# Performance work log

Measured on AMD Instinct MI355X. Metric: run time of the kernel, lower is better.

The kernel has to match this reference:

```python
import jax, jax.numpy as jnp
import numpy as np

SOS_TOKEN = 1
MAX_LENGTH = 64
VOCAB = 32000
HIDDEN = 1024
BATCH = 32


def setup_inputs() -> dict:
    key = jax.random.key(0)
    ks = jax.random.split(key, 10)
    s = 1.0 / np.sqrt(HIDDEN)
    return {
        "encoder_outputs": jax.random.normal(ks[0], (BATCH, MAX_LENGTH, HIDDEN), dtype=jnp.float32),
        "encoder_hidden": jax.random.normal(ks[1], (1, BATCH, HIDDEN), dtype=jnp.float32),
        "target_tensor": jax.random.randint(ks[2], (BATCH, MAX_LENGTH), 0, VOCAB),
        "embedding": jax.random.normal(ks[3], (VOCAB, HIDDEN), dtype=jnp.float32),
        "W_ih": jax.random.uniform(ks[4], (3 * HIDDEN, HIDDEN), jnp.float32, -s, s),
        "W_hh": jax.random.uniform(ks[5], (3 * HIDDEN, HIDDEN), jnp.float32, -s, s),
        "b_ih": jax.random.uniform(ks[6], (3 * HIDDEN,), jnp.float32, -s, s),
        "b_hh": jax.random.uniform(ks[7], (3 * HIDDEN,), jnp.float32, -s, s),
        "out_W": jax.random.uniform(ks[8], (VOCAB, HIDDEN), jnp.float32, -s, s),
        "out_b": jax.random.uniform(ks[9], (VOCAB,), jnp.float32, -s, s),
    }


def _decode(encoder_hidden, target_tensor, embedding, W_ih, W_hh, b_ih, b_hh, out_W, out_b):
    B = target_tensor.shape[0]
    # teacher forcing: input at step i is SOS (i=0) else target[:, i-1]
    sos = jnp.full((B, 1), SOS_TOKEN, dtype=target_tensor.dtype)
    inputs = jnp.concatenate([sos, target_tensor[:, :-1]], axis=1)  # [B,T]
    x = jax.nn.relu(embedding[inputs])  # [B,T,H]
    # precompute all input-side gate projections in one GEMM: [B,T,3H]
    xg = jnp.einsum("bth,gh->btg", x, W_ih) + b_ih
    h0 = encoder_hidden[0]  # [B,H]

    def step(h, xg_t):
        hg = h @ W_hh.T + b_hh  # [B,3H]
        xr, xz, xn = jnp.split(xg_t, 3, axis=-1)
        hr, hz, hn = jnp.split(hg, 3, axis=-1)
        r = jax.nn.sigmoid(xr + hr)
        z = jax.nn.sigmoid(xz + hz)
        n = jnp.tanh(xn + r * hn)
        h_new = (1.0 - z) * n + z * h
        return h_new, h_new

    h_last, hs = jax.lax.scan(step, h0, jnp.swapaxes(xg, 0, 1))
    hs = jnp.swapaxes(hs, 0, 1)  # [B,T,H]
    logits = jnp.einsum("bth,vh->btv", hs, out_W) + out_b
    log_probs = jax.nn.log_softmax(logits, axis=-1)
    return log_probs, h_last[None]  # hidden shaped [1,B,H] like torch GRU


def reference(encoder_outputs, encoder_hidden, target_tensor, embedding, W_ih, W_hh, b_ih, b_hh, out_W, out_b):
    del encoder_outputs  # only used for batch size in the original
    return _decode(encoder_hidden, target_tensor, embedding, W_ih, W_hh, b_ih, b_hh, out_W, out_b)
```

## Files before the change

### kernel.cpp

```cpp
#include <hip/hip_runtime.h>
#include <hip/hip_bf16.h>

#define B_ 32
#define T_ 64
#define H_ 1024
#define G3 3072
#define V_ 32000
#define M_ 2048
#define NB_SCAN 64
#define NTILE_N 250

typedef __attribute__((ext_vector_type(8))) short s16x8;
typedef __attribute__((ext_vector_type(4))) float f32x4;
typedef __bf16 bf16x8 __attribute__((ext_vector_type(8)));

__device__ inline unsigned short f2bf(float f) {
    union { float f; unsigned int u; } v; v.f = f;
    unsigned int u = v.u;
    return (unsigned short)((u + 0x7FFFu + ((u >> 16) & 1u)) >> 16);
}

__device__ inline s16x8 load_b128_cc(const void* p) {
    s16x8 r;
    asm volatile("global_load_dwordx4 %0, %1, off sc0 sc1" : "=v"(r) : "v"(p));
    return r;
}
__device__ inline unsigned int load_b32_cc(const void* p) {
    unsigned int r;
    asm volatile("global_load_dword %0, %1, off sc0 sc1" : "=v"(r) : "v"(p));
    return r;
}
__device__ inline void store_b32_cc(void* p, unsigned int v) {
    asm volatile("global_store_dword %0, %1, off sc0 sc1" :: "v"(p), "v"(v) : "memory");
}

__global__ __launch_bounds__(256) void prep_all(
    const float* __restrict__ W_ih, const float* __restrict__ W_hh,
    const float* __restrict__ out_W,
    unsigned short* __restrict__ wihb, unsigned short* __restrict__ whhb,
    unsigned short* __restrict__ owb,
    const int* __restrict__ target, const float* __restrict__ emb,
    unsigned short* __restrict__ xb,
    const float* __restrict__ enc_hidden, unsigned short* __restrict__ hb0,
    unsigned int* __restrict__ flg)
{
    int gid = blockIdx.x * 256 + threadIdx.x;
    int gs = gridDim.x * 256;
    const int NW = G3 * H_ / 4;
    const int NO = V_ * H_ / 4;

    for (int i = gid; i < NW; i += gs) {
        float4 v = *(const float4*)(W_ih + (size_t)i * 4);
        ushort4 o; o.x = f2bf(v.x); o.y = f2bf(v.y); o.z = f2bf(v.z); o.w = f2bf(v.w);
        *(ushort4*)(wihb + (size_t)i * 4) = o;
    }
    for (int i = gid; i < NW; i += gs) {
        float4 v = *(const float4*)(W_hh + (size_t)i * 4);
        ushort4 o; o.x = f2bf(v.x); o.y = f2bf(v.y); o.z = f2bf(v.z); o.w = f2bf(v.w);
        *(ushort4*)(whhb + (size_t)i * 4) = o;
    }
    for (int i = gid; i < NO; i += gs) {
        float4 v = *(const float4*)(out_W + (size_t)i * 4);
        ushort4 o; o.x = f2bf(v.x); o.y = f2bf(v.y); o.z = f2bf(v.z); o.w = f2bf(v.w);
        *(ushort4*)(owb + (size_t)i * 4) = o;
    }
    for (int i = gid; i < M_ * 256; i += gs) {
        int m = i >> 8, k = (i & 255) * 4;
        int b = m >> 6, t = m & 63;
        int tok = (t == 0) ? 1 : target[b * T_ + t - 1];
        float4 v = *(const float4*)(emb + (size_t)tok * H_ + k);
        ushort4 o;
        o.x = f2bf(fmaxf(v.x, 0.f)); o.y = f2bf(fmaxf(v.y, 0.f));
        o.z = f2bf(fmaxf(v.z, 0.f)); o.w = f2bf(fmaxf(v.w, 0.f));
        *(ushort4*)(xb + (size_t)m * H_ + k) = o;
    }
    for (int i = gid; i < B_ * H_; i += gs) hb0[i] = f2bf(enc_hidden[i]);
    for (int i = gid; i < 128; i += gs) flg[i] = 0;
}

__global__ __launch_bounds__(256) void gemm_bias(
    const unsigned short* __restrict__ A,
    const unsigned short* __restrict__ Bm,
    const float* __restrict__ bias,
    float* __restrict__ C,
    int N, int K)
{
    __shared__ __align__(16) unsigned short As[3 * 4096];
    __shared__ __align__(16) unsigned short Bs[3 * 4096];
    int n0 = blockIdx.x * 128, m0 = blockIdx.y * 128;
    int tid = threadIdx.x;
    int lane = tid & 63, wv = tid >> 6;
    int wr = wv >> 1, wc = wv & 1;

    f32x4 acc[4][4] = {};

    int o0 = wv * 2048 + lane * 16;
    int row0 = o0 >> 6, sl0 = (o0 >> 4) & 3;
    int ib0 = (sl0 ^ ((row0 >> 1) & 3)) * 8;
    int o1 = o0 + 1024;
    int row1 = o1 >> 6, sl1 = (o1 >> 4) & 3;
    int ib1 = (sl1 ^ ((row1 >> 1) & 3)) * 8;

    auto stage = [&](int buf, int k0) {
        const unsigned short* ga0 = A + (size_t)(m0 + row0) * K + k0 + ib0;
        const unsigned short* gb0 = Bm + (size_t)(n0 + row0) * K + k0 + ib0;
        const unsigned short* ga1 = A + (size_t)(m0 + row1) * K + k0 + ib1;
        const unsigned short* gb1 = Bm + (size_t)(n0 + row1) * K + k0 + ib1;
        unsigned short* la0 = As + buf * 4096 + wv * 1024;
        unsigned short* lb0 = Bs + buf * 4096 + wv * 1024;
        __builtin_amdgcn_global_load_lds((const __attribute__((address_space(1))) void*)ga0,
                                         (__attribute__((address_space(3))) void*)la0, 16, 0, 0);
        __builtin_amdgcn_global_load_lds((const __attribute__((address_space(1))) void*)gb0,
                                         (__attribute__((address_space(3))) void*)lb0, 16, 0, 0);
        __builtin_amdgcn_global_load_lds((const __attribute__((address_space(1))) void*)ga1,
                                         (__attribute__((address_space(3))) void*)(la0 + 512), 16, 0, 0);
        __builtin_amdgcn_global_load_lds((const __attribute__((address_space(1))) void*)gb1,
                                         (__attribute__((address_space(3))) void*)(lb0 + 512), 16, 0, 0);
    };

    int rr2 = lane & 15, q = lane >> 4;
    int kqs = ((q ^ ((rr2 >> 1) & 3)) * 8);
    int rA = wr * 64 + rr2;
    int rB = wc * 64 + rr2;

    int NT = K >> 5;
    stage(0, 0);
    if (NT > 1) {
        stage(1, 32);
        asm volatile("s_waitcnt vmcnt(4)");
    } else {
        asm volatile("s_waitcnt vmcnt(0)");
    }
    __builtin_amdgcn_s_barrier();
    __builtin_amdgcn_sched_barrier(0);

    int cur = 0;
    for (int t = 0; t < NT; ++t) {
        if (t + 2 < NT) {
            int nb = cur + 2; if (nb >= 3) nb -= 3;
            stage(nb, (t + 2) << 5);
        }
        const unsigned short* ab = As + cur * 4096;
        const unsigned short* bb = Bs + cur * 4096;
        s16x8 af[4], bf[4];
#pragma unroll
        for (int i = 0; i < 4; ++i) {
            af[i] = *(const s16x8*)(ab + (rA + i * 16) * 32 + kqs);
            bf[i] = *(const s16x8*)(bb + (rB + i * 16) * 32 + kqs);
        }
#pragma unroll
        for (int mf = 0; mf < 4; ++mf)
#pragma unroll
            for (int nf = 0; nf < 4; ++nf)
                acc[mf][nf] = __builtin_amdgcn_mfma_f32_16x16x32_bf16(
                    __builtin_bit_cast(bf16x8, af[mf]),
                    __builtin_bit_cast(bf16x8, bf[nf]),
                    acc[mf][nf], 0, 0, 0);
        if (t + 1 < NT) {
            if (t + 2 < NT) asm volatile("s_waitcnt vmcnt(4)");
            else            asm volatile("s_waitcnt vmcnt(0)");
            asm volatile("s_waitcnt lgkmcnt(0)");
            __builtin_amdgcn_s_barrier();
            __builtin_amdgcn_sched_barrier(0);
        }
        cur = (cur == 2) ? 0 : cur + 1;
    }

#pragma unroll
    for (int nf = 0; nf < 4; ++nf) {
        int col = n0 + wc * 64 + nf * 16 + rr2;
        float bv = bias[col];
#pragma unroll
        for (int mf = 0; mf < 4; ++mf) {
            int mbase = m0 + wr * 64 + mf * 16 + q * 4;
#pragma unroll
            for (int r = 0; r < 4; ++r)
                C[(size_t)(mbase + r) * N + col] = acc[mf][nf][r] + bv;
        }
    }
}

__global__ __launch_bounds__(256) void gemm_logits(
    const unsigned short* __restrict__ A,
    const unsigned short* __restrict__ Bm,
    const float* __restrict__ bias,
    float* __restrict__ C,
    float* __restrict__ pmax,
    float* __restrict__ psum)
{
    __shared__ __align__(16) unsigned short As[3 * 4096];
    __shared__ __align__(16) unsigned short Bs[3 * 4096];
    __shared__ float spx[2][128], sps[2][128];
    int m0 = blockIdx.x * 128;
    int ntile = blockIdx.y;
    int n0 = ntile * 128;
    int tid = threadIdx.x;
    int lane = tid & 63, wv = tid >> 6;
    int wr = wv >> 1, wc = wv & 1;

    f32x4 acc[4][4] = {};

    int o0 = wv * 2048 + lane * 16;
    int row0 = o0 >> 6, sl0 = (o0 >> 4) & 3;
    int ib0 = (sl0 ^ ((row0 >> 1) & 3)) * 8;
    int o1 = o0 + 1024;
    int row1 = o1 >> 6, sl1 = (o1 >> 4) & 3;
    int ib1 = (sl1 ^ ((row1 >> 1) & 3)) * 8;

    auto stage = [&](int buf, int k0) {
        const unsigned short* ga0 = A + (size_t)(m0 + row0) * H_ + k0 + ib0;
        const unsigned short* gb0 = Bm + (size_t)(n0 + row0) * H_ + k0 + ib0;
        const unsigned short* ga1 = A + (size_t)(m0 + row1) * H_ + k0 + ib1;
        const unsigned short* gb1 = Bm + (size_t)(n0 + row1) * H_ + k0 + ib1;
        unsigned short* la0 = As + buf * 4096 + wv * 1024;
        unsigned short* lb0 = Bs + buf * 4096 + wv * 1024;
        __builtin_amdgcn_global_load_lds((const __attribute__((address_space(1))) void*)ga0,
                                         (__attribute__((address_space(3))) void*)la0, 16, 0, 0);
        __builtin_amdgcn_global_load_lds((const __attribute__((address_space(1))) void*)gb0,
                                         (__attribute__((address_space(3))) void*)lb0, 16, 0, 0);
        __builtin_amdgcn_global_load_lds((const __attribute__((address_space(1))) void*)ga1,
                                         (__attribute__((address_space(3))) void*)(la0 + 512), 16, 0, 0);
        __builtin_amdgcn_global_load_lds((const __attribute__((address_space(1))) void*)gb1,
                                         (__attribute__((address_space(3))) void*)(lb0 + 512), 16, 0, 0);
    };

    int q = lane >> 4, rr2 = lane & 15;
    int kqs = ((q ^ ((rr2 >> 1) & 3)) * 8);
    int rA = wr * 64 + rr2;
    int rB = wc * 64 + rr2;

    stage(0, 0);
    stage(1, 32);
    asm volatile("s_waitcnt vmcnt(4)");
    __builtin_amdgcn_s_barrier();
    __builtin_amdgcn_sched_barrier(0);

    int cur = 0;
    for (int t = 0; t < 32; ++t) {
        if (t + 2 < 32) {
            int nb = cur + 2; if (nb >= 3) nb -= 3;
            stage(nb, (t + 2) << 5);
        }
        const unsigned short* ab = As + cur * 4096;
        const unsigned short* bb = Bs + cur * 4096;
        s16x8 af[4], bf[4];
#pragma unroll
        for (int i = 0; i < 4; ++i) {
            af[i] = *(const s16x8*)(ab + (rA + i * 16) * 32 + kqs);
            bf[i] = *(const s16x8*)(bb + (rB + i * 16) * 32 + kqs);
        }
#pragma unroll
        for (int mf = 0; mf < 4; ++mf)
#pragma unroll
            for (int nf = 0; nf < 4; ++nf)
                acc[mf][nf] = __builtin_amdgcn_mfma_f32_16x16x32_bf16(
                    __builtin_bit_cast(bf16x8, af[mf]),
                    __builtin_bit_cast(bf16x8, bf[nf]),
                    acc[mf][nf], 0, 0, 0);
        if (t + 1 < 32) {
            if (t + 2 < 32) asm volatile("s_waitcnt vmcnt(4)");
            else            asm volatile("s_waitcnt vmcnt(0)");
            asm volatile("s_waitcnt lgkmcnt(0)");
            __builtin_amdgcn_s_barrier();
            __builtin_amdgcn_sched_barrier(0);
        }
        cur = (cur == 2) ? 0 : cur + 1;
    }

    float bv[4];
#pragma unroll
    for (int nf = 0; nf < 4; ++nf) bv[nf] = bias[n0 + wc * 64 + nf * 16 + rr2];

#pragma unroll
    for (int mf = 0; mf < 4; ++mf) {
#pragma unroll
        for (int r = 0; r < 4; ++r) {
            int row_local = wr * 64 + mf * 16 + q * 4 + r;
            float vmax = -1e30f;
#pragma unroll
            for (int nf = 0; nf < 4; ++nf) vmax = fmaxf(vmax, acc[mf][nf][r] + bv[nf]);
#pragma unroll
            for (int o = 1; o < 16; o <<= 1) vmax = fmaxf(vmax, __shfl_xor(vmax, o));
            float vsum = 0.f;
#pragma unroll
            for (int nf = 0; nf < 4; ++nf) vsum += __expf(acc[mf][nf][r] + bv[nf] - vmax);
#pragma unroll
            for (int o = 1; o < 16; o <<= 1) vsum += __shfl_xor(vsum, o);
            if (rr2 == 0) { spx[wc][row_local] = vmax; sps[wc][row_local] = vsum; }
        }
    }

#pragma unroll
    for (int nf = 0; nf < 4; ++nf) {
        int col = n0 + wc * 64 + nf * 16 + rr2;
#pragma unroll
        for (int mf = 0; mf < 4; ++mf) {
            int mbase = m0 + wr * 64 + mf * 16 + q * 4;
#pragma unroll
            for (int r = 0; r < 4; ++r)
                C[(size_t)(mbase + r) * V_ + col] = acc[mf][nf][r] + bv[nf];
        }
    }

    __syncthreads();
    if (wc == 0 && rr2 == 0) {
#pragma unroll
        for (int mf = 0; mf < 4; ++mf)
#pragma unroll
            for (int r = 0; r < 4; ++r) {
                int row_local = wr * 64 + mf * 16 + q * 4 + r;
                float m0v = spx[0][row_local], m1v = spx[1][row_local];
                float Mv = fmaxf(m0v, m1v);
                float Sv = sps[0][row_local] * __expf(m0v - Mv) + sps[1][row_local] * __expf(m1v - Mv);
                pmax[(size_t)(m0 + row_local) * NTILE_N + ntile] = Mv;
                psum[(size_t)(m0 + row_local) * NTILE_N + ntile] = Sv;
            }
    }
}

__global__ __launch_bounds__(256) void gru_scan(
    const unsigned short* __restrict__ Whhb,
    const float* __restrict__ b_hh,
    const float* __restrict__ enc_hidden,
    const float* __restrict__ xg,
    unsigned short* __restrict__ hb0, unsigned short* __restrict__ hb1,
    float* __restrict__ hfF,
    unsigned short* __restrict__ hs,
    unsigned int* __restrict__ flags)
{
    __shared__ __align__(16) unsigned short ws_[48 * 1024];
    __shared__ __align__(16) f32x4 red[2][3][64];

    int tid = threadIdx.x;
    int lane = tid & 63, wave = tid >> 6;
    int rt = wave >> 1, kh = wave & 1;
    int ct = blockIdx.x;

    for (int idx = tid; idx < 48 * 128; idx += 256) {
        int r = idx >> 7, slot = idx & 127;
        int g = r >> 4, jr = r & 15;
        s16x8 v = *(const s16x8*)(Whhb + (size_t)(g * H_ + ct * 16 + jr) * H_ + slot * 8);
        *(s16x8*)(ws_ + r * 1024 + (slot ^ (r & 7)) * 8) = v;
    }
    __syncthreads();

    int rr = lane & 15, q = lane >> 4;
    int col = ct * 16 + rr;
    int xsw = rr & 7;
    int kbase = kh * 512;
    int sbase = kh * 64 + q;
    float br = b_hh[col], bz = b_hh[H_ + col], bn = b_hh[2 * H_ + col];
    int b0 = rt * 16 + q * 4;

    float hold[4];
    float xr[4], xz[4], xn[4];
    if (kh == 1) {
#pragma unroll
        for (int r = 0; r < 4; ++r) {
            hold[r] = enc_hidden[(b0 + r) * H_ + col];
            const float* xrow = xg + ((size_t)(b0 + r) * T_) * G3;
            xr[r] = xrow[col]; xz[r] = xrow[H_ + col]; xn[r] = xrow[2 * H_ + col];
        }
    }

    for (int t = 0; t < T_; ++t) {
        const unsigned short* hbp = (t & 1) ? hb1 : hb0;
        unsigned short*       hbn = (t & 1) ? hb0 : hb1;

        const unsigned short* ha = hbp + (size_t)(rt * 16 + rr) * H_ + kbase + q * 8;
        s16x8 af[16];
#pragma unroll
        for (int i = 0; i < 16; ++i) af[i] = load_b128_cc(ha + i * 32);

        f32x4 accr, accz, accn;
        if (kh == 1) {
            accr = (f32x4){br, br, br, br};
            accz = (f32x4){bz, bz, bz, bz};
            accn = (f32x4){bn, bn, bn, bn};
        } else {
            accr = (f32x4){0.f, 0.f, 0.f, 0.f};
            accz = accr; accn = accr;
        }

        asm volatile("s_waitcnt vmcnt(0)");
        __builtin_amdgcn_sched_barrier(0);

#pragma unroll
        for (int kk = 0; kk < 16; ++kk) {
            int so = ((sbase + kk * 4) ^ xsw) * 8;
            s16x8 fr = *(const s16x8*)(ws_ + rr * 1024 + so);
            s16x8 fz = *(const s16x8*)(ws_ + (16 + rr) * 1024 + so);
            s16x8 fn = *(const s16x8*)(ws_ + (32 + rr) * 1024 + so);
            bf16x8 a = __builtin_bit_cast(bf16x8, af[kk]);
            accr = __builtin_amdgcn_mfma_f32_16x16x32_bf16(a, __builtin_bit_cast(bf16x8, fr), accr, 0, 0, 0);
            accz = __builtin_amdgcn_mfma_f32_16x16x32_bf16(a, __builtin_bit_cast(bf16x8, fz), accz, 0, 0, 0);
            accn = __builtin_amdgcn_mfma_f32_16x16x32_bf16(a, __builtin_bit_cast(bf16x8, fn), accn, 0, 0, 0);
        }

        if (kh == 0) {
            red[rt][0][lane] = accr; red[rt][1][lane] = accz; red[rt][2][lane] = accn;
        }
        __syncthreads();
        if (kh == 1) {
            accr += red[rt][0][lane]; accz += red[rt][1][lane]; accn += red[rt][2][lane];
            unsigned int hpk[4];
#pragma unroll
            for (int r = 0; r < 4; ++r) {
                float rg = 1.f / (1.f + __expf(-(xr[r] + accr[r])));
                float zg = 1.f / (1.f + __expf(-(xz[r] + accz[r])));
                float ng = tanhf(xn[r] + rg * accn[r]);
                float hnew = (1.f - zg) * ng + zg * hold[r];
                hold[r] = hnew;
                hpk[r] = f2bf(hnew);
            }
#pragma unroll
            for (int r = 0; r < 4; ++r) {
                unsigned int other = __shfl_xor((int)hpk[r], 1);
                if ((rr & 1) == 0) {
                    unsigned int pk = hpk[r] | (other << 16);
                    store_b32_cc(hbn + (size_t)(b0 + r) * H_ + col, pk);
                    *(unsigned int*)(hs + ((size_t)(b0 + r) * T_ + t) * H_ + col) = pk;
                }
            }
            if (t == T_ - 1) {
#pragma unroll
                for (int r = 0; r < 4; ++r) hfF[(b0 + r) * H_ + col] = hold[r];
            }
            asm volatile("s_waitcnt vmcnt(0)" ::: "memory");
        }

        if (t < T_ - 1) {
            __syncthreads();
            if (tid == 0) store_b32_cc(flags + ct, (unsigned int)(t + 1));
            if (kh == 1) {
#pragma unroll
                for (int r = 0; r < 4; ++r) {
                    const float* xrow = xg + ((size_t)(b0 + r) * T_ + (t + 1)) * G3;
                    xr[r] = xrow[col]; xz[r] = xrow[H_ + col]; xn[r] = xrow[2 * H_ + col];
                }
                __builtin_amdgcn_sched_barrier(0);
            }
            unsigned int tgt = (unsigned int)(t + 1);
            while (true) {
                unsigned int f = load_b32_cc(flags + lane);
                asm volatile("s_waitcnt vmcnt(0)");
                if (__all(f >= tgt)) break;
                __builtin_amdgcn_s_sleep(1);
            }
            __builtin_amdgcn_sched_barrier(0);
        }
    }
}

__global__ __launch_bounds__(256) void lse_sub_copy(
    float* __restrict__ out,
    const float* __restrict__ pmax, const float* __restrict__ psum,
    const float* __restrict__ hfF)
{
    int m = blockIdx.x;
    int tid = threadIdx.x;
    __shared__ float sm[4], ssum[4];

    if (m < B_) {
        float4 v = *(const float4*)(hfF + m * H_ + tid * 4);
        *(float4*)(out + (size_t)M_ * V_ + m * H_ + tid * 4) = v;
    }

    float M = -1e30f, S = 0.f;
    for (int i = tid; i < NTILE_N; i += 256) {
        float pm_ = pmax[(size_t)m * NTILE_N + i];
        float ps_ = psum[(size_t)m * NTILE_N + i];
        float nm = fmaxf(M, pm_);
        S = S * __expf(M - nm) + ps_ * __expf(pm_ - nm);
        M = nm;
    }
    for (int o = 32; o > 0; o >>= 1) {
        float om = __shfl_xor(M, o), os = __shfl_xor(S, o);
        float nm = fmaxf(M, om);
        S = S * __expf(M - nm) + os * __expf(om - nm);
        M = nm;
    }
    int wv = tid >> 6, lane = tid & 63;
    if (lane == 0) { sm[wv] = M; ssum[wv] = S; }
    __syncthreads();
    float fm = fmaxf(fmaxf(sm[0], sm[1]), fmaxf(sm[2], sm[3]));
    float fs = ssum[0] * __expf(sm[0] - fm) + ssum[1] * __expf(sm[1] - fm)
             + ssum[2] * __expf(sm[2] - fm) + ssum[3] * __expf(sm[3] - fm);
    float lse = fm + __logf(fs);

    float* row = out + (size_t)m * V_;
    for (int i = tid * 4; i < V_; i += 1024) {
        float4 v = *(const float4*)(row + i);
        v.x -= lse; v.y -= lse; v.z -= lse; v.w -= lse;
        *(float4*)(row + i) = v;
    }
}

extern "C" void kernel_launch(void* const* d_in, const int* in_sizes, int n_in,
                              void* d_out, int out_size, void* d_ws, size_t ws_size,
                              hipStream_t stream) {
    const float* enc_hidden = (const float*)d_in[1];
    const int*   target     = (const int*)d_in[2];
    const float* embedding  = (const float*)d_in[3];
    const float* W_ih       = (const float*)d_in[4];
    const float* W_hh       = (const float*)d_in[5];
    const float* b_ih       = (const float*)d_in[6];
    const float* b_hh       = (const float*)d_in[7];
    const float* out_W      = (const float*)d_in[8];
    const float* out_b      = (const float*)d_in[9];
    float* out = (float*)d_out;

    char* ws = (char*)d_ws;
    float*          xg   = (float*)(ws);
    unsigned short* xb   = (unsigned short*)(ws + 25165824);
    unsigned short* hsb  = (unsigned short*)(ws + 29360128);
    unsigned short* wihb = (unsigned short*)(ws + 33554432);
    unsigned short* whhb = (unsigned short*)(ws + 39845888);
    unsigned short* owb  = (unsigned short*)(ws + 46137344);
    float*          hfF  = (float*)(ws + 111673344);
    unsigned short* hb0  = (unsigned short*)(ws + 111804416);
    unsigned short* hb1  = (unsigned short*)(ws + 111869952);
    unsigned int*   flg  = (unsigned int*)(ws + 111935488);
    float*          pmx  = (float*)(ws + 25165824);
    float*          psm  = (float*)(ws + 25165824 + 2048000);

    prep_all<<<2048, 256, 0, stream>>>(W_ih, W_hh, out_W, wihb, whhb, owb,
                                       target, embedding, xb, enc_hidden, hb0, flg);

    gemm_bias<<<dim3(G3 / 128, M_ / 128), 256, 0, stream>>>(xb, wihb, b_ih, xg, G3, H_);

    {
        void* args[] = { (void*)&whhb, (void*)&b_hh, (void*)&enc_hidden, (void*)&xg,
                         (void*)&hb0, (void*)&hb1, (void*)&hfF, (void*)&hsb, (void*)&flg };
        hipLaunchCooperativeKernel((const void*)gru_scan, dim3(NB_SCAN), dim3(256), args, 0, stream);
    }

    gemm_logits<<<dim3(M_ / 128, NTILE_N), 256, 0, stream>>>(hsb, owb, out_b, out, pmx, psm);

    lse_sub_copy<<<M_, 256, 0, stream>>>(out, pmx, psm, hfF);
}
```

Measured before the change: 889.6 us.

## Enlarge logits GEMM tile to 256x256 with 8 waves and split-phase pipeline

The logits GEMM moves from 128x128 tiles with 4 waves to 256x256 tiles with 8 waves and a K-step of 64. LDS is double-buffered, and staging is interleaved across four MFMA sub-phases with s_setprio raised around the MFMA blocks. The aim is more data reuse per loaded byte and less barrier overhead in the dominant vocab projection. The cost is 128 KB of LDS and more accumulator registers per block, which limits occupancy, plus fewer blocks overall. The GRU scan also swaps the inline-asm coherent store for a relaxed agent-scope atomic exchange.

Measured after the change: 828.0 us (median of 2 runs). 6.9% less time.

```diff
diff --git a/kernel.cpp b/kernel.cpp
--- a/kernel.cpp
+++ b/kernel.cpp
@@ -8,7 +8,8 @@
 #define V_ 32000
 #define M_ 2048
 #define NB_SCAN 64
-#define NTILE_N 250
+#define NKT 16
+#define NTN2 125
 
 typedef __attribute__((ext_vector_type(8))) short s16x8;
 typedef __attribute__((ext_vector_type(4))) float f32x4;
@@ -18,6 +19,11 @@
     union { float f; unsigned int u; } v; v.f = f;
     unsigned int u = v.u;
     return (unsigned short)((u + 0x7FFFu + ((u >> 16) & 1u)) >> 16);
+}
+
+__device__ inline f32x4 mfma16(s16x8 a, s16x8 b, f32x4 c) {
+    return __builtin_amdgcn_mfma_f32_16x16x32_bf16(
+        __builtin_bit_cast(bf16x8, a), __builtin_bit_cast(bf16x8, b), c, 0, 0, 0);
 }
 
 __device__ inline s16x8 load_b128_cc(const void* p) {
@@ -152,10 +158,7 @@
         for (int mf = 0; mf < 4; ++mf)
 #pragma unroll
             for (int nf = 0; nf < 4; ++nf)
-                acc[mf][nf] = __builtin_amdgcn_mfma_f32_16x16x32_bf16(
-                    __builtin_bit_cast(bf16x8, af[mf]),
-                    __builtin_bit_cast(bf16x8, bf[nf]),
-                    acc[mf][nf], 0, 0, 0);
+                acc[mf][nf] = mfma16(af[mf], bf[nf], acc[mf][nf]);
         if (t + 1 < NT) {
             if (t + 2 < NT) asm volatile("s_waitcnt vmcnt(4)");
             else            asm volatile("s_waitcnt vmcnt(0)");
@@ -180,7 +183,7 @@
     }
 }
 
-__global__ __launch_bounds__(256) void gemm_logits(
+__global__ __launch_bounds__(512) void gemm_logits(
     const unsigned short* __restrict__ A,
     const unsigned short* __restrict__ Bm,
     const float* __restrict__ bias,
@@ -188,83 +191,108 @@
     float* __restrict__ pmax,
     float* __restrict__ psum)
 {
-    __shared__ __align__(16) unsigned short As[3 * 4096];
-    __shared__ __align__(16) unsigned short Bs[3 * 4096];
-    __shared__ float spx[2][128], sps[2][128];
-    int m0 = blockIdx.x * 128;
+    __shared__ __align__(16) unsigned short lds[65536];
+    __shared__ float spx[4][256], sps[4][256];
+
+    int m0 = blockIdx.x * 256;
     int ntile = blockIdx.y;
-    int n0 = ntile * 128;
+    int n0 = ntile * 256;
     int tid = threadIdx.x;
     int lane = tid & 63, wv = tid >> 6;
-    int wr = wv >> 1, wc = wv & 1;
-
-    f32x4 acc[4][4] = {};
-
-    int o0 = wv * 2048 + lane * 16;
-    int row0 = o0 >> 6, sl0 = (o0 >> 4) & 3;
-    int ib0 = (sl0 ^ ((row0 >> 1) & 3)) * 8;
-    int o1 = o0 + 1024;
-    int row1 = o1 >> 6, sl1 = (o1 >> 4) & 3;
-    int ib1 = (sl1 ^ ((row1 >> 1) & 3)) * 8;
-
-    auto stage = [&](int buf, int k0) {
-        const unsigned short* ga0 = A + (size_t)(m0 + row0) * H_ + k0 + ib0;
-        const unsigned short* gb0 = Bm + (size_t)(n0 + row0) * H_ + k0 + ib0;
-        const unsigned short* ga1 = A + (size_t)(m0 + row1) * H_ + k0 + ib1;
-        const unsigned short* gb1 = Bm + (size_t)(n0 + row1) * H_ + k0 + ib1;
-        unsigned short* la0 = As + buf * 4096 + wv * 1024;
-        unsigned short* lb0 = Bs + buf * 4096 + wv * 1024;
-        __builtin_amdgcn_global_load_lds((const __attribute__((address_space(1))) void*)ga0,
-                                         (__attribute__((address_space(3))) void*)la0, 16, 0, 0);
-        __builtin_amdgcn_global_load_lds((const __attribute__((address_space(1))) void*)gb0,
-                                         (__attribute__((address_space(3))) void*)lb0, 16, 0, 0);
-        __builtin_amdgcn_global_load_lds((const __attribute__((address_space(1))) void*)ga1,
-                                         (__attribute__((address_space(3))) void*)(la0 + 512), 16, 0, 0);
-        __builtin_amdgcn_global_load_lds((const __attribute__((address_space(1))) void*)gb1,
-                                         (__attribute__((address_space(3))) void*)(lb0 + 512), 16, 0, 0);
+    int wr = wv >> 2, wc = wv & 3;
+    int q = lane >> 4, rr2 = lane & 15;
+    int swz = rr2 & 7;
+
+    int srow = tid >> 3;
+    int scol = ((tid & 7) ^ (srow & 7)) * 8;
+
+    f32x4 acc[8][4] = {};
+
+    auto stage_unit = [&](int slot, const unsigned short* gb, int grow0, int kc) {
+        const unsigned short* src = gb + (size_t)(grow0 + srow) * H_ + kc + scol;
+        unsigned short* dst = lds + slot * 4096 + wv * 512;
+        __builtin_amdgcn_global_load_lds((const __attribute__((address_space(1))) void*)src,
+                                         (__attribute__((address_space(3))) void*)dst, 16, 0, 0);
     };
 
-    int q = lane >> 4, rr2 = lane & 15;
-    int kqs = ((q ^ ((rr2 >> 1) & 3)) * 8);
-    int rA = wr * 64 + rr2;
-    int rB = wc * 64 + rr2;
-
-    stage(0, 0);
-    stage(1, 32);
-    asm volatile("s_waitcnt vmcnt(4)");
-    __builtin_amdgcn_s_barrier();
-    __builtin_amdgcn_sched_barrier(0);
-
-    int cur = 0;
-    for (int t = 0; t < 32; ++t) {
-        if (t + 2 < 32) {
-            int nb = cur + 2; if (nb >= 3) nb -= 3;
-            stage(nb, (t + 2) << 5);
-        }
-        const unsigned short* ab = As + cur * 4096;
-        const unsigned short* bb = Bs + cur * 4096;
-        s16x8 af[4], bf[4];
+    stage_unit(0, Bm, n0,       0);
+    stage_unit(1, Bm, n0 + 64,  0);
+    stage_unit(2, Bm, n0 + 128, 0);
+    stage_unit(3, Bm, n0 + 192, 0);
+    stage_unit(4, A,  m0,       0);
+    stage_unit(5, A,  m0 + 128, 0);
+    stage_unit(6, A,  m0 + 64,  0);
+    stage_unit(7, A,  m0 + 192, 0);
+
+    for (int kt = 0; kt < NKT; ++kt) {
+        int sb  = (kt & 1) ? 32768 : 0;
+        int nsb = (kt & 1) ? 0 : 8;
+        int A0 = sb + (4 + wr) * 4096;
+        int A1 = sb + (6 + wr) * 4096;
+        int Bb = sb + wc * 4096;
+        int k1 = (kt + 1) << 6;
+        bool more = (kt + 1 < NKT);
+
+        s16x8 bf0[4], bf1[4], af[4];
+
+        asm volatile("s_waitcnt vmcnt(2)");
+        __builtin_amdgcn_s_barrier();
+        __builtin_amdgcn_sched_barrier(0);
+        if (more) { stage_unit(nsb + 0, Bm, n0, k1); stage_unit(nsb + 1, Bm, n0 + 64, k1); }
 #pragma unroll
         for (int i = 0; i < 4; ++i) {
-            af[i] = *(const s16x8*)(ab + (rA + i * 16) * 32 + kqs);
-            bf[i] = *(const s16x8*)(bb + (rB + i * 16) * 32 + kqs);
-        }
-#pragma unroll
-        for (int mf = 0; mf < 4; ++mf)
+            bf0[i] = *(const s16x8*)(lds + Bb + (i * 16 + rr2) * 64 + (q ^ swz) * 8);
+            af[i]  = *(const s16x8*)(lds + A0 + (i * 16 + rr2) * 64 + (q ^ swz) * 8);
+        }
+        __builtin_amdgcn_s_setprio(1);
+#pragma unroll
+        for (int i = 0; i < 4; ++i)
 #pragma unroll
             for (int nf = 0; nf < 4; ++nf)
-                acc[mf][nf] = __builtin_amdgcn_mfma_f32_16x16x32_bf16(
-                    __builtin_bit_cast(bf16x8, af[mf]),
-                    __builtin_bit_cast(bf16x8, bf[nf]),
-                    acc[mf][nf], 0, 0, 0);
-        if (t + 1 < 32) {
-            if (t + 2 < 32) asm volatile("s_waitcnt vmcnt(4)");
-            else            asm volatile("s_waitcnt vmcnt(0)");
-            asm volatile("s_waitcnt lgkmcnt(0)");
-            __builtin_amdgcn_s_barrier();
-            __builtin_amdgcn_sched_barrier(0);
-        }
-        cur = (cur == 2) ? 0 : cur + 1;
+                acc[i][nf] = mfma16(af[i], bf0[nf], acc[i][nf]);
+        __builtin_amdgcn_s_setprio(0);
+
+        if (more) asm volatile("s_waitcnt vmcnt(2)");
+        else      asm volatile("s_waitcnt vmcnt(0)");
+        __builtin_amdgcn_s_barrier();
+        __builtin_amdgcn_sched_barrier(0);
+        if (more) { stage_unit(nsb + 2, Bm, n0 + 128, k1); stage_unit(nsb + 3, Bm, n0 + 192, k1); }
+#pragma unroll
+        for (int i = 0; i < 4; ++i)
+            af[i] = *(const s16x8*)(lds + A1 + (i * 16 + rr2) * 64 + (q ^ swz) * 8);
+        __builtin_amdgcn_s_setprio(1);
+#pragma unroll
+        for (int i = 0; i < 4; ++i)
+#pragma unroll
+            for (int nf = 0; nf < 4; ++nf)
+                acc[4 + i][nf] = mfma16(af[i], bf0[nf], acc[4 + i][nf]);
+        __builtin_amdgcn_s_setprio(0);
+
+        if (more) { stage_unit(nsb + 4, A, m0, k1); stage_unit(nsb + 5, A, m0 + 128, k1); }
+#pragma unroll
+        for (int i = 0; i < 4; ++i) {
+            bf1[i] = *(const s16x8*)(lds + Bb + (i * 16 + rr2) * 64 + ((4 + q) ^ swz) * 8);
+            af[i]  = *(const s16x8*)(lds + A0 + (i * 16 + rr2) * 64 + ((4 + q) ^ swz) * 8);
+        }
+        __builtin_amdgcn_s_setprio(1);
+#pragma unroll
+        for (int i = 0; i < 4; ++i)
+#pragma unroll
+            for (int nf = 0; nf < 4; ++nf)
+                acc[i][nf] = mfma16(af[i], bf1[nf], acc[i][nf]);
+        __builtin_amdgcn_s_setprio(0);
+
+        if (more) { stage_unit(nsb + 6, A, m0 + 64, k1); stage_unit(nsb + 7, A, m0 + 192, k1); }
+#pragma unroll
+        for (int i = 0; i < 4; ++i)
+            af[i] = *(const s16x8*)(lds + A1 + (i * 16 + rr2) * 64 + ((4 + q) ^ swz) * 8);
+        __builtin_amdgcn_s_setprio(1);
+#pragma unroll
+        for (int i = 0; i < 4; ++i)
+#pragma unroll
+            for (int nf = 0; nf < 4; ++nf)
+                acc[4 + i][nf] = mfma16(af[i], bf1[nf], acc[4 + i][nf]);
+        __builtin_amdgcn_s_setprio(0);
     }
 
     float bv[4];
@@ -272,10 +300,10 @@
     for (int nf = 0; nf < 4; ++nf) bv[nf] = bias[n0 + wc * 64 + nf * 16 + rr2];
 
 #pragma unroll
-    for (int mf = 0; mf < 4; ++mf) {
+    for (int mf = 0; mf < 8; ++mf) {
 #pragma unroll
         for (int r = 0; r < 4; ++r) {
-            int row_local = wr * 64 + mf * 16 + q * 4 + r;
+            int row_local = wr * 128 + mf * 16 + q * 4 + r;
             float vmax = -1e30f;
 #pragma unroll
             for (int nf = 0; nf < 4; ++nf) vmax = fmaxf(vmax, acc[mf][nf][r] + bv[nf]);
@@ -294,8 +322,8 @@
     for (int nf = 0; nf < 4; ++nf) {
         int col = n0 + wc * 64 + nf * 16 + rr2;
 #pragma unroll
-        for (int mf = 0; mf < 4; ++mf) {
-            int mbase = m0 + wr * 64 + mf * 16 + q * 4;
+        for (int mf = 0; mf < 8; ++mf) {
+            int mbase = m0 + wr * 128 + mf * 16 + q * 4;
 #pragma unroll
             for (int r = 0; r < 4; ++r)
                 C[(size_t)(mbase + r) * V_ + col] = acc[mf][nf][r] + bv[nf];
@@ -303,18 +331,14 @@
     }
 
     __syncthreads();
-    if (wc == 0 && rr2 == 0) {
-#pragma unroll
-        for (int mf = 0; mf < 4; ++mf)
-#pragma unroll
-            for (int r = 0; r < 4; ++r) {
-                int row_local = wr * 64 + mf * 16 + q * 4 + r;
-                float m0v = spx[0][row_local], m1v = spx[1][row_local];
-                float Mv = fmaxf(m0v, m1v);
-                float Sv = sps[0][row_local] * __expf(m0v - Mv) + sps[1][row_local] * __expf(m1v - Mv);
-                pmax[(size_t)(m0 + row_local) * NTILE_N + ntile] = Mv;
-                psum[(size_t)(m0 + row_local) * NTILE_N + ntile] = Sv;
-            }
+    if (tid < 256) {
+        int row = tid;
+        float m0v = spx[0][row], m1v = spx[1][row], m2v = spx[2][row], m3v = spx[3][row];
+        float Mv = fmaxf(fmaxf(m0v, m1v), fmaxf(m2v, m3v));
+        float Sv = sps[0][row] * __expf(m0v - Mv) + sps[1][row] * __expf(m1v - Mv)
+                 + sps[2][row] * __expf(m2v - Mv) + sps[3][row] * __expf(m3v - Mv);
+        pmax[(size_t)(m0 + row) * NTN2 + ntile] = Mv;
+        psum[(size_t)(m0 + row) * NTN2 + ntile] = Sv;
     }
 }
 
@@ -391,10 +415,9 @@
             s16x8 fr = *(const s16x8*)(ws_ + rr * 1024 + so);
             s16x8 fz = *(const s16x8*)(ws_ + (16 + rr) * 1024 + so);
             s16x8 fn = *(const s16x8*)(ws_ + (32 + rr) * 1024 + so);
-            bf16x8 a = __builtin_bit_cast(bf16x8, af[kk]);
-            accr = __builtin_amdgcn_mfma_f32_16x16x32_bf16(a, __builtin_bit_cast(bf16x8, fr), accr, 0, 0, 0);
-            accz = __builtin_amdgcn_mfma_f32_16x16x32_bf16(a, __builtin_bit_cast(bf16x8, fz), accz, 0, 0, 0);
-            accn = __builtin_amdgcn_mfma_f32_16x16x32_bf16(a, __builtin_bit_cast(bf16x8, fn), accn, 0, 0, 0);
+            accr = mfma16(af[kk], fr, accr);
+            accz = mfma16(af[kk], fz, accz);
+            accn = mfma16(af[kk], fn, accn);
         }
 
         if (kh == 0) {
@@ -418,7 +441,8 @@
                 unsigned int other = __shfl_xor((int)hpk[r], 1);
                 if ((rr & 1) == 0) {
                     unsigned int pk = hpk[r] | (other << 16);
-                    store_b32_cc(hbn + (size_t)(b0 + r) * H_ + col, pk);
+                    unsigned int* dst = (unsigned int*)(hbn + (size_t)(b0 + r) * H_ + col);
+                    (void)__hip_atomic_exchange(dst, pk, __ATOMIC_RELAXED, __HIP_MEMORY_SCOPE_AGENT);
                     *(unsigned int*)(hs + ((size_t)(b0 + r) * T_ + t) * H_ + col) = pk;
                 }
             }
@@ -467,9 +491,9 @@
     }
 
     float M = -1e30f, S = 0.f;
-    for (int i = tid; i < NTILE_N; i += 256) {
-        float pm_ = pmax[(size_t)m * NTILE_N + i];
-        float ps_ = psum[(size_t)m * NTILE_N + i];
+    for (int i = tid; i < NTN2; i += 256) {
+        float pm_ = pmax[(size_t)m * NTN2 + i];
+        float ps_ = psum[(size_t)m * NTN2 + i];
         float nm = fmaxf(M, pm_);
         S = S * __expf(M - nm) + ps_ * __expf(pm_ - nm);
         M = nm;
@@ -535,7 +559,7 @@
         hipLaunchCooperativeKernel((const void*)gru_scan, dim3(NB_SCAN), dim3(256), args, 0, stream);
     }
 
-    gemm_logits<<<dim3(M_ / 128, NTILE_N), 256, 0, stream>>>(hsb, owb, out_b, out, pmx, psm);
+    gemm_logits<<<dim3(M_ / 256, NTN2), 512, 0, stream>>>(hsb, owb, out_b, out, pmx, psm);
 
     lse_sub_copy<<<M_, 256, 0, stream>>>(out, pmx, psm, hfF);
 }
```

## Fuse GRU scan with logits GEMM in one cooperative kernel using flag-gated tiles

Applied to the files above, without the earlier changes.

Merges the recurrent scan and the output-projection GEMM into one cooperative launch of 256 blocks. 64 blocks run the scan while the others compute logits tiles as soon as the flags show the needed timesteps are done. hs is stored time-major so each 128-row tile maps to four timesteps, and output rows are remapped back to batch-major. The goal is to hide the serial scan latency behind GEMM work. In exchange the logits GEMM drops to double buffering with A loaded through registers and no LDS swizzle, and only 192 blocks work on it during the scan.

Result: faster. 831.9 us (-6.5%).

```diff
diff --git a/kernel.cpp b/kernel.cpp
--- a/kernel.cpp
+++ b/kernel.cpp
@@ -8,7 +8,10 @@
 #define V_ 32000
 #define M_ 2048
 #define NB_SCAN 64
+#define NB_ALL 256
 #define NTILE_N 250
+#define NTILE_ALL 4000
+#define NTILE_MAIN 3500
 
 typedef __attribute__((ext_vector_type(8))) short s16x8;
 typedef __attribute__((ext_vector_type(4))) float f32x4;
@@ -18,6 +21,11 @@
     union { float f; unsigned int u; } v; v.f = f;
     unsigned int u = v.u;
     return (unsigned short)((u + 0x7FFFu + ((u >> 16) & 1u)) >> 16);
+}
+
+__device__ inline f32x4 mfma16(s16x8 a, s16x8 b, f32x4 c) {
+    return __builtin_amdgcn_mfma_f32_16x16x32_bf16(
+        __builtin_bit_cast(bf16x8, a), __builtin_bit_cast(bf16x8, b), c, 0, 0, 0);
 }
 
 __device__ inline s16x8 load_b128_cc(const void* p) {
@@ -152,10 +160,7 @@
         for (int mf = 0; mf < 4; ++mf)
 #pragma unroll
             for (int nf = 0; nf < 4; ++nf)
-                acc[mf][nf] = __builtin_amdgcn_mfma_f32_16x16x32_bf16(
-                    __builtin_bit_cast(bf16x8, af[mf]),
-                    __builtin_bit_cast(bf16x8, bf[nf]),
-                    acc[mf][nf], 0, 0, 0);
+                acc[mf][nf] = mfma16(af[mf], bf[nf], acc[mf][nf]);
         if (t + 1 < NT) {
             if (t + 2 < NT) asm volatile("s_waitcnt vmcnt(4)");
             else            asm volatile("s_waitcnt vmcnt(0)");
@@ -180,96 +185,105 @@
     }
 }
 
-__global__ __launch_bounds__(256) void gemm_logits(
-    const unsigned short* __restrict__ A,
-    const unsigned short* __restrict__ Bm,
-    const float* __restrict__ bias,
-    float* __restrict__ C,
-    float* __restrict__ pmax,
-    float* __restrict__ psum)
+__device__ __forceinline__ void logits_tile(
+    const unsigned short* __restrict__ hs,
+    const unsigned short* __restrict__ owb,
+    const float* __restrict__ out_b,
+    float* __restrict__ out,
+    unsigned int* __restrict__ flags,
+    unsigned short* As, unsigned short* Bs,
+    float (*spx)[128], float (*sps)[128],
+    float* __restrict__ pmax, float* __restrict__ psum,
+    int tau)
 {
-    __shared__ __align__(16) unsigned short As[3 * 4096];
-    __shared__ __align__(16) unsigned short Bs[3 * 4096];
-    __shared__ float spx[2][128], sps[2][128];
-    int m0 = blockIdx.x * 128;
-    int ntile = blockIdx.y;
-    int n0 = ntile * 128;
     int tid = threadIdx.x;
     int lane = tid & 63, wv = tid >> 6;
     int wr = wv >> 1, wc = wv & 1;
+    int q = lane >> 4, rr2 = lane & 15;
+    int tg_t = tau / NTILE_N, tg_n = tau - tg_t * NTILE_N;
+    int m0 = tg_t << 7, n0 = tg_n << 7;
+
+    unsigned tgt = (unsigned)(tg_t * 4 + 4);
+    while (true) {
+        unsigned f = load_b32_cc(flags + lane);
+        asm volatile("s_waitcnt vmcnt(0)");
+        if (__all(f >= tgt)) break;
+        __builtin_amdgcn_s_sleep(16);
+    }
+    __builtin_amdgcn_sched_barrier(0);
+
+    const unsigned short* At = hs + (size_t)m0 * H_;
+    const unsigned short* Bt = owb + (size_t)n0 * H_;
 
     f32x4 acc[4][4] = {};
 
     int o0 = wv * 2048 + lane * 16;
-    int row0 = o0 >> 6, sl0 = (o0 >> 4) & 3;
-    int ib0 = (sl0 ^ ((row0 >> 1) & 3)) * 8;
+    int row0 = o0 >> 6, ib0 = (o0 & 63) >> 1;
     int o1 = o0 + 1024;
-    int row1 = o1 >> 6, sl1 = (o1 >> 4) & 3;
-    int ib1 = (sl1 ^ ((row1 >> 1) & 3)) * 8;
-
-    auto stage = [&](int buf, int k0) {
-        const unsigned short* ga0 = A + (size_t)(m0 + row0) * H_ + k0 + ib0;
-        const unsigned short* gb0 = Bm + (size_t)(n0 + row0) * H_ + k0 + ib0;
-        const unsigned short* ga1 = A + (size_t)(m0 + row1) * H_ + k0 + ib1;
-        const unsigned short* gb1 = Bm + (size_t)(n0 + row1) * H_ + k0 + ib1;
-        unsigned short* la0 = As + buf * 4096 + wv * 1024;
+    int row1 = o1 >> 6, ib1 = (o1 & 63) >> 1;
+    int d0 = o0 >> 1, d1 = o1 >> 1;
+
+    auto stageB = [&](int buf, int k0) {
+        const unsigned short* gb0 = Bt + (size_t)row0 * H_ + k0 + ib0;
+        const unsigned short* gb1 = Bt + (size_t)row1 * H_ + k0 + ib1;
         unsigned short* lb0 = Bs + buf * 4096 + wv * 1024;
-        __builtin_amdgcn_global_load_lds((const __attribute__((address_space(1))) void*)ga0,
-                                         (__attribute__((address_space(3))) void*)la0, 16, 0, 0);
         __builtin_amdgcn_global_load_lds((const __attribute__((address_space(1))) void*)gb0,
                                          (__attribute__((address_space(3))) void*)lb0, 16, 0, 0);
-        __builtin_amdgcn_global_load_lds((const __attribute__((address_space(1))) void*)ga1,
-                                         (__attribute__((address_space(3))) void*)(la0 + 512), 16, 0, 0);
         __builtin_amdgcn_global_load_lds((const __attribute__((address_space(1))) void*)gb1,
                                          (__attribute__((address_space(3))) void*)(lb0 + 512), 16, 0, 0);
     };
-
-    int q = lane >> 4, rr2 = lane & 15;
-    int kqs = ((q ^ ((rr2 >> 1) & 3)) * 8);
+    auto loadA = [&](int k0, s16x8& a0, s16x8& a1) {
+        a0 = load_b128_cc(At + (size_t)row0 * H_ + k0 + ib0);
+        a1 = load_b128_cc(At + (size_t)row1 * H_ + k0 + ib1);
+    };
+
+    int kq = q * 8;
     int rA = wr * 64 + rr2;
     int rB = wc * 64 + rr2;
 
-    stage(0, 0);
-    stage(1, 32);
-    asm volatile("s_waitcnt vmcnt(4)");
-    __builtin_amdgcn_s_barrier();
-    __builtin_amdgcn_sched_barrier(0);
+    {
+        s16x8 a0, a1;
+        loadA(0, a0, a1);
+        stageB(0, 0);
+        asm volatile("s_waitcnt vmcnt(0)" ::: "memory");
+        __builtin_amdgcn_sched_barrier(0);
+        *(s16x8*)(As + d0) = a0;
+        *(s16x8*)(As + d1) = a1;
+    }
+    __syncthreads();
 
     int cur = 0;
+#pragma unroll 1
     for (int t = 0; t < 32; ++t) {
-        if (t + 2 < 32) {
-            int nb = cur + 2; if (nb >= 3) nb -= 3;
-            stage(nb, (t + 2) << 5);
-        }
+        s16x8 na0, na1;
+        bool more = (t + 1 < 32);
+        if (more) { loadA((t + 1) << 5, na0, na1); stageB(cur ^ 1, (t + 1) << 5); }
         const unsigned short* ab = As + cur * 4096;
         const unsigned short* bb = Bs + cur * 4096;
         s16x8 af[4], bf[4];
 #pragma unroll
         for (int i = 0; i < 4; ++i) {
-            af[i] = *(const s16x8*)(ab + (rA + i * 16) * 32 + kqs);
-            bf[i] = *(const s16x8*)(bb + (rB + i * 16) * 32 + kqs);
+            af[i] = *(const s16x8*)(ab + (rA + i * 16) * 32 + kq);
+            bf[i] = *(const s16x8*)(bb + (rB + i * 16) * 32 + kq);
         }
 #pragma unroll
         for (int mf = 0; mf < 4; ++mf)
 #pragma unroll
             for (int nf = 0; nf < 4; ++nf)
-                acc[mf][nf] = __builtin_amdgcn_mfma_f32_16x16x32_bf16(
-                    __builtin_bit_cast(bf16x8, af[mf]),
-                    __builtin_bit_cast(bf16x8, bf[nf]),
-                    acc[mf][nf], 0, 0, 0);
-        if (t + 1 < 32) {
-            if (t + 2 < 32) asm volatile("s_waitcnt vmcnt(4)");
-            else            asm volatile("s_waitcnt vmcnt(0)");
-            asm volatile("s_waitcnt lgkmcnt(0)");
-            __builtin_amdgcn_s_barrier();
+                acc[mf][nf] = mfma16(af[mf], bf[nf], acc[mf][nf]);
+        if (more) {
+            asm volatile("s_waitcnt vmcnt(0)" ::: "memory");
             __builtin_amdgcn_sched_barrier(0);
-        }
-        cur = (cur == 2) ? 0 : cur + 1;
+            *(s16x8*)(As + (cur ^ 1) * 4096 + d0) = na0;
+            *(s16x8*)(As + (cur ^ 1) * 4096 + d1) = na1;
+        }
+        __syncthreads();
+        cur ^= 1;
     }
 
     float bv[4];
 #pragma unroll
-    for (int nf = 0; nf < 4; ++nf) bv[nf] = bias[n0 + wc * 64 + nf * 16 + rr2];
+    for (int nf = 0; nf < 4; ++nf) bv[nf] = out_b[n0 + wc * 64 + nf * 16 + rr2];
 
 #pragma unroll
     for (int mf = 0; mf < 4; ++mf) {
@@ -295,10 +309,13 @@
         int col = n0 + wc * 64 + nf * 16 + rr2;
 #pragma unroll
         for (int mf = 0; mf < 4; ++mf) {
-            int mbase = m0 + wr * 64 + mf * 16 + q * 4;
-#pragma unroll
-            for (int r = 0; r < 4; ++r)
-                C[(size_t)(mbase + r) * V_ + col] = acc[mf][nf][r] + bv[nf];
+            int mloc = wr * 64 + mf * 16 + q * 4;
+#pragma unroll
+            for (int r = 0; r < 4; ++r) {
+                int mp = m0 + mloc + r;
+                int orow = ((mp & 31) << 6) | (mp >> 5);
+                out[(size_t)orow * V_ + col] = acc[mf][nf][r] + bv[nf];
+            }
         }
     }
 
@@ -309,16 +326,19 @@
 #pragma unroll
             for (int r = 0; r < 4; ++r) {
                 int row_local = wr * 64 + mf * 16 + q * 4 + r;
+                int mp = m0 + row_local;
+                int orow = ((mp & 31) << 6) | (mp >> 5);
                 float m0v = spx[0][row_local], m1v = spx[1][row_local];
                 float Mv = fmaxf(m0v, m1v);
                 float Sv = sps[0][row_local] * __expf(m0v - Mv) + sps[1][row_local] * __expf(m1v - Mv);
-                pmax[(size_t)(m0 + row_local) * NTILE_N + ntile] = Mv;
-                psum[(size_t)(m0 + row_local) * NTILE_N + ntile] = Sv;
-            }
-    }
-}
-
-__global__ __launch_bounds__(256) void gru_scan(
+                pmax[(size_t)orow * NTILE_N + tg_n] = Mv;
+                psum[(size_t)orow * NTILE_N + tg_n] = Sv;
+            }
+    }
+    __syncthreads();
+}
+
+__global__ __launch_bounds__(256, 1) void fused_scan_logits(
     const unsigned short* __restrict__ Whhb,
     const float* __restrict__ b_hh,
     const float* __restrict__ enc_hidden,
@@ -326,130 +346,153 @@
     unsigned short* __restrict__ hb0, unsigned short* __restrict__ hb1,
     float* __restrict__ hfF,
     unsigned short* __restrict__ hs,
-    unsigned int* __restrict__ flags)
+    unsigned int* __restrict__ flags,
+    const unsigned short* __restrict__ owb,
+    const float* __restrict__ out_b,
+    float* __restrict__ out,
+    float* __restrict__ pmax, float* __restrict__ psum)
 {
-    __shared__ __align__(16) unsigned short ws_[48 * 1024];
-    __shared__ __align__(16) f32x4 red[2][3][64];
+    __shared__ __align__(16) char smem[104448];
+    unsigned short* As = (unsigned short*)smem;
+    unsigned short* Bs = (unsigned short*)(smem + 16384);
+    float (*spx)[128] = (float (*)[128])(smem + 32768);
+    float (*sps)[128] = (float (*)[128])(smem + 32768 + 1024);
 
     int tid = threadIdx.x;
-    int lane = tid & 63, wave = tid >> 6;
-    int rt = wave >> 1, kh = wave & 1;
-    int ct = blockIdx.x;
-
-    for (int idx = tid; idx < 48 * 128; idx += 256) {
-        int r = idx >> 7, slot = idx & 127;
-        int g = r >> 4, jr = r & 15;
-        s16x8 v = *(const s16x8*)(Whhb + (size_t)(g * H_ + ct * 16 + jr) * H_ + slot * 8);
-        *(s16x8*)(ws_ + r * 1024 + (slot ^ (r & 7)) * 8) = v;
-    }
-    __syncthreads();
-
-    int rr = lane & 15, q = lane >> 4;
-    int col = ct * 16 + rr;
-    int xsw = rr & 7;
-    int kbase = kh * 512;
-    int sbase = kh * 64 + q;
-    float br = b_hh[col], bz = b_hh[H_ + col], bn = b_hh[2 * H_ + col];
-    int b0 = rt * 16 + q * 4;
-
-    float hold[4];
-    float xr[4], xz[4], xn[4];
-    if (kh == 1) {
-#pragma unroll
-        for (int r = 0; r < 4; ++r) {
-            hold[r] = enc_hidden[(b0 + r) * H_ + col];
-            const float* xrow = xg + ((size_t)(b0 + r) * T_) * G3;
-            xr[r] = xrow[col]; xz[r] = xrow[H_ + col]; xn[r] = xrow[2 * H_ + col];
-        }
-    }
-
-    for (int t = 0; t < T_; ++t) {
-        const unsigned short* hbp = (t & 1) ? hb1 : hb0;
-        unsigned short*       hbn = (t & 1) ? hb0 : hb1;
-
-        const unsigned short* ha = hbp + (size_t)(rt * 16 + rr) * H_ + kbase + q * 8;
-        s16x8 af[16];
-#pragma unroll
-        for (int i = 0; i < 16; ++i) af[i] = load_b128_cc(ha + i * 32);
-
-        f32x4 accr, accz, accn;
+    int bid = blockIdx.x;
+
+    if (bid < NB_SCAN) {
+        unsigned short* ws_ = (unsigned short*)smem;
+        f32x4 (*red)[3][64] = (f32x4 (*)[3][64])(smem + 98304);
+
+        int lane = tid & 63, wave = tid >> 6;
+        int rt = wave >> 1, kh = wave & 1;
+        int ct = bid;
+
+        for (int idx = tid; idx < 48 * 128; idx += 256) {
+            int r = idx >> 7, slot = idx & 127;
+            int g = r >> 4, jr = r & 15;
+            s16x8 v = *(const s16x8*)(Whhb + (size_t)(g * H_ + ct * 16 + jr) * H_ + slot * 8);
+            *(s16x8*)(ws_ + r * 1024 + (slot ^ (r & 7)) * 8) = v;
+        }
+        __syncthreads();
+
+        int rr = lane & 15, q = lane >> 4;
+        int col = ct * 16 + rr;
+        int xsw = rr & 7;
+        int kbase = kh * 512;
+        int sbase = kh * 64 + q;
+        float br = b_hh[col], bz = b_hh[H_ + col], bn = b_hh[2 * H_ + col];
+        int b0 = rt * 16 + q * 4;
+
+        float hold[4];
+        float xr[4], xz[4], xn[4];
         if (kh == 1) {
-            accr = (f32x4){br, br, br, br};
-            accz = (f32x4){bz, bz, bz, bz};
-            accn = (f32x4){bn, bn, bn, bn};
-        } else {
-            accr = (f32x4){0.f, 0.f, 0.f, 0.f};
-            accz = accr; accn = accr;
-        }
-
-        asm volatile("s_waitcnt vmcnt(0)");
-        __builtin_amdgcn_sched_barrier(0);
-
-#pragma unroll
-        for (int kk = 0; kk < 16; ++kk) {
-            int so = ((sbase + kk * 4) ^ xsw) * 8;
-            s16x8 fr = *(const s16x8*)(ws_ + rr * 1024 + so);
-            s16x8 fz = *(const s16x8*)(ws_ + (16 + rr) * 1024 + so);
-            s16x8 fn = *(const s16x8*)(ws_ + (32 + rr) * 1024 + so);
-            bf16x8 a = __builtin_bit_cast(bf16x8, af[kk]);
-            accr = __builtin_amdgcn_mfma_f32_16x16x32_bf16(a, __builtin_bit_cast(bf16x8, fr), accr, 0, 0, 0);
-            accz = __builtin_amdgcn_mfma_f32_16x16x32_bf16(a, __builtin_bit_cast(bf16x8, fz), accz, 0, 0, 0);
-            accn = __builtin_amdgcn_mfma_f32_16x16x32_bf16(a, __builtin_bit_cast(bf16x8, fn), accn, 0, 0, 0);
-        }
-
-        if (kh == 0) {
-            red[rt][0][lane] = accr; red[rt][1][lane] = accz; red[rt][2][lane] = accn;
-        }
-        __syncthreads();
-        if (kh == 1) {
-            accr += red[rt][0][lane]; accz += red[rt][1][lane]; accn += red[rt][2][lane];
-            unsigned int hpk[4];
 #pragma unroll
             for (int r = 0; r < 4; ++r) {
-                float rg = 1.f / (1.f + __expf(-(xr[r] + accr[r])));
-                float zg = 1.f / (1.f + __expf(-(xz[r] + accz[r])));
-                float ng = tanhf(xn[r] + rg * accn[r]);
-                float hnew = (1.f - zg) * ng + zg * hold[r];
-                hold[r] = hnew;
-                hpk[r] = f2bf(hnew);
-            }
-#pragma unroll
-            for (int r = 0; r < 4; ++r) {
-                unsigned int other = __shfl_xor((int)hpk[r], 1);
-                if ((rr & 1) == 0) {
-                    unsigned int pk = hpk[r] | (other << 16);
-                    store_b32_cc(hbn + (size_t)(b0 + r) * H_ + col, pk);
-                    *(unsigned int*)(hs + ((size_t)(b0 + r) * T_ + t) * H_ + col) = pk;
+                hold[r] = enc_hidden[(b0 + r) * H_ + col];
+                const float* xrow = xg + ((size_t)(b0 + r) * T_) * G3;
+                xr[r] = xrow[col]; xz[r] = xrow[H_ + col]; xn[r] = xrow[2 * H_ + col];
+            }
+        }
+
+        for (int t = 0; t < T_; ++t) {
+            const unsigned short* hbp = (t & 1) ? hb1 : hb0;
+            unsigned short*       hbn = (t & 1) ? hb0 : hb1;
+
+            const unsigned short* ha = hbp + (size_t)(rt * 16 + rr) * H_ + kbase + q * 8;
+            s16x8 af[16];
+#pragma unroll
+            for (int i = 0; i < 16; ++i) af[i] = load_b128_cc(ha + i * 32);
+
+            f32x4 accr, accz, accn;
+            if (kh == 1) {
+                accr = (f32x4){br, br, br, br};
+                accz = (f32x4){bz, bz, bz, bz};
+                accn = (f32x4){bn, bn, bn, bn};
+            } else {
+                accr = (f32x4){0.f, 0.f, 0.f, 0.f};
+                accz = accr; accn = accr;
+            }
+
+            asm volatile("s_waitcnt vmcnt(0)");
+            __builtin_amdgcn_sched_barrier(0);
+
+#pragma unroll
+            for (int kk = 0; kk < 16; ++kk) {
+                int so = ((sbase + kk * 4) ^ xsw) * 8;
+                s16x8 fr = *(const s16x8*)(ws_ + rr * 1024 + so);
+                s16x8 fz = *(const s16x8*)(ws_ + (16 + rr) * 1024 + so);
+                s16x8 fn = *(const s16x8*)(ws_ + (32 + rr) * 1024 + so);
+                accr = mfma16(af[kk], fr, accr);
+                accz = mfma16(af[kk], fz, accz);
+                accn = mfma16(af[kk], fn, accn);
+            }
+
+            if (kh == 0) {
+                red[rt][0][lane] = accr; red[rt][1][lane] = accz; red[rt][2][lane] = accn;
+            }
+            __syncthreads();
+            if (kh == 1) {
+                accr += red[rt][0][lane]; accz += red[rt][1][lane]; accn += red[rt][2][lane];
+                unsigned int hpk[4];
+#pragma unroll
+                for (int r = 0; r < 4; ++r) {
+                    float rg = 1.f / (1.f + __expf(-(xr[r] + accr[r])));
+                    float zg = 1.f / (1.f + __expf(-(xz[r] + accz[r])));
+                    float ng = tanhf(xn[r] + rg * accn[r]);
+                    float hnew = (1.f - zg) * ng + zg * hold[r];
+                    hold[r] = hnew;
+                    hpk[r] = f2bf(hnew);
                 }
-            }
-            if (t == T_ - 1) {
-#pragma unroll
-                for (int r = 0; r < 4; ++r) hfF[(b0 + r) * H_ + col] = hold[r];
-            }
-            asm volatile("s_waitcnt vmcnt(0)" ::: "memory");
-        }
-
-        if (t < T_ - 1) {
+#pragma unroll
+                for (int r = 0; r < 4; ++r) {
+                    unsigned int other = __shfl_xor((int)hpk[r], 1);
+                    if ((rr & 1) == 0) {
+                        unsigned int pk = hpk[r] | (other << 16);
+                        unsigned int* hd = (unsigned int*)(hbn + (size_t)(b0 + r) * H_ + col);
+                        (void)__hip_atomic_exchange(hd, pk, __ATOMIC_RELAXED, __HIP_MEMORY_SCOPE_AGENT);
+                        unsigned int* sd = (unsigned int*)(hs + ((size_t)t * B_ + (b0 + r)) * H_ + col);
+                        (void)__hip_atomic_exchange(sd, pk, __ATOMIC_RELAXED, __HIP_MEMORY_SCOPE_AGENT);
+                    }
+                }
+                if (t == T_ - 1) {
+#pragma unroll
+                    for (int r = 0; r < 4; ++r) hfF[(b0 + r) * H_ + col] = hold[r];
+                }
+                asm volatile("s_waitcnt vmcnt(0)" ::: "memory");
+            }
+
             __syncthreads();
             if (tid == 0) store_b32_cc(flags + ct, (unsigned int)(t + 1));
-            if (kh == 1) {
-#pragma unroll
-                for (int r = 0; r < 4; ++r) {
-                    const float* xrow = xg + ((size_t)(b0 + r) * T_ + (t + 1)) * G3;
-                    xr[r] = xrow[col]; xz[r] = xrow[H_ + col]; xn[r] = xrow[2 * H_ + col];
+
+            if (t < T_ - 1) {
+                if (kh == 1) {
+#pragma unroll
+                    for (int r = 0; r < 4; ++r) {
+                        const float* xrow = xg + ((size_t)(b0 + r) * T_ + (t + 1)) * G3;
+                        xr[r] = xrow[col]; xz[r] = xrow[H_ + col]; xn[r] = xrow[2 * H_ + col];
+                    }
+                    __builtin_amdgcn_sched_barrier(0);
+                }
+                unsigned int tgt = (unsigned int)(t + 1);
+                while (true) {
+                    unsigned int f = load_b32_cc(flags + lane);
+                    asm volatile("s_waitcnt vmcnt(0)");
+                    if (__all(f >= tgt)) break;
+                    __builtin_amdgcn_s_sleep(1);
                 }
                 __builtin_amdgcn_sched_barrier(0);
             }
-            unsigned int tgt = (unsigned int)(t + 1);
-            while (true) {
-                unsigned int f = load_b32_cc(flags + lane);
-                asm volatile("s_waitcnt vmcnt(0)");
-                if (__all(f >= tgt)) break;
-                __builtin_amdgcn_s_sleep(1);
-            }
-            __builtin_amdgcn_sched_barrier(0);
-        }
-    }
+        }
+        __syncthreads();
+    } else {
+        for (int tau = bid - NB_SCAN; tau < NTILE_MAIN; tau += (NB_ALL - NB_SCAN))
+            logits_tile(hs, owb, out_b, out, flags, As, Bs, spx, sps, pmax, psum, tau);
+    }
+
+    for (int tau = NTILE_MAIN + bid; tau < NTILE_ALL; tau += NB_ALL)
+        logits_tile(hs, owb, out_b, out, flags, As, Bs, spx, sps, pmax, psum, tau);
 }
 
 __global__ __launch_bounds__(256) void lse_sub_copy(
@@ -531,11 +574,10 @@
 
     {
         void* args[] = { (void*)&whhb, (void*)&b_hh, (void*)&enc_hidden, (void*)&xg,
-                         (void*)&hb0, (void*)&hb1, (void*)&hfF, (void*)&hsb, (void*)&flg };
-        hipLaunchCooperativeKernel((const void*)gru_scan, dim3(NB_SCAN), dim3(256), args, 0, stream);
-    }
-
-    gemm_logits<<<dim3(M_ / 128, NTILE_N), 256, 0, stream>>>(hsb, owb, out_b, out, pmx, psm);
+                         (void*)&hb0, (void*)&hb1, (void*)&hfF, (void*)&hsb, (void*)&flg,
+                         (void*)&owb, (void*)&out_b, (void*)&out, (void*)&pmx, (void*)&psm };
+        hipLaunchCooperativeKernel((const void*)fused_scan_logits, dim3(NB_ALL), dim3(256), args, 0, stream);
+    }
 
     lse_sub_copy<<<M_, 256, 0, stream>>>(out, pmx, psm, hfF);
 }
```
